# Kernel optimization log

Hardware: AMD Instinct MI355X
Metric: run time of the kernel (lower is better)

## Reference

```python
import jax, jax.numpy as jnp
import numpy as np

B, NA, NB, DF, H, DO, NT = 32, 128, 1024, 128, 512, 128, 5
NPAIR = NT * NT  # nn_index = z1*5 + z2 -> 25 pair-type MLPs


def setup_inputs() -> dict:
    key = jax.random.key(0)
    ks = jax.random.split(key, 6)
    z = jax.random.randint(ks[0], (B, NA), 0, NT)
    r = jax.random.normal(ks[1], (B, NA, 3), jnp.float32) * 5.0
    x = jax.random.normal(ks[2], (B, NA, DF), jnp.float32)
    t = jax.random.randint(ks[3], (B, NB, 2), 0, NA)
    pad = NB // 8  # last 1/8 of bonds are -1 padding, as in the torch module
    t = t.at[:, NB - pad:, :].set(-1)
    # Stacked per-pair-type 2-layer MLP params (map_list)
    W1 = jax.random.normal(ks[4], (NPAIR, 2 * DF, H), jnp.float32) / np.sqrt(2.0 * DF)
    b1 = jnp.zeros((NPAIR, H), jnp.float32)
    W2 = jax.random.normal(ks[5], (NPAIR, H, DO), jnp.float32) / np.sqrt(1.0 * H)
    b2 = jnp.zeros((NPAIR, DO), jnp.float32)
    return dict(z=z, r=r, x=x, t=t, W1=W1, b1=b1, W2=W2, b2=b2)


def reference(z, r, x, t, W1, b1, W2, b2):
    n_batch, n_bonds, _ = t.shape
    n_atoms = x.shape[1]
    x_f = x.reshape(-1, x.shape[-1])          # [B*NA, DF]
    z_f = z.reshape(-1)                        # [B*NA]
    r_f = r.reshape(-1, 3)                     # [B*NA, 3]
    offs = (jnp.arange(n_batch) * n_atoms)[:, None, None]
    valid = t[:, :, 0] != -1                   # [B, NB]
    tg = jnp.clip(t, 0, None) + offs           # global atom indices (padding clamped to 0)
    t1 = tg[:, :, 0].reshape(-1)
    t2 = tg[:, :, 1].reshape(-1)
    vmask = valid.reshape(-1)                  # [N] = [B*NB]
    # gather+concat pair features; zero out padded rows (masked_scatter into zeros)
    x_c = jnp.concatenate([x_f[t1], x_f[t2]], axis=1) * vmask[:, None].astype(x.dtype)
    z1 = z_f[t1]
    z2 = z_f[t2]
    nn_index = jnp.where(vmask, z1 * NT + z2, -1)
    # per-pair-type MLP dispatch (loop over fixed 25 types; rows selected by mask)
    y = jnp.zeros((x_c.shape[0], W2.shape[-1]), x.dtype)
    for i in range(NPAIR):
        h = jax.nn.silu(x_c @ W1[i] + b1[i])
        out_i = h @ W2[i] + b2[i]
        y = jnp.where((nn_index == i)[:, None], out_i, y)
    y = y.reshape(n_batch, n_bonds, -1)
    # normalized bond vectors, zeroed for padded bonds
    v = (r_f[t2] - r_f[t1]).reshape(n_batch, n_bonds, 3)
    n2 = jnp.sum(v * v, axis=2, keepdims=True)
    v = v / jnp.sqrt(jnp.clip(n2, 1e-24, None))  # == clamp(norm, 1e-12)
    v = v * valid[:, :, None].astype(v.dtype)
    return (z, x, t, y, v)
```

## Files before the change

### kernel.cpp

```cpp
#include <hip/hip_runtime.h>
#include <cstddef>
#include <cstdint>

#define NBATCH 32
#define NATOM  128
#define DFEAT  128
#define HDIM   512
#define DOUT   128
#define NTYPE  5
#define NPAIR  25
#define NBOND  32768
#define CAP    1408
#define TPT    22
#define GBLK   550

#define OFF_X 4096
#define OFF_T 528384
#define OFF_Y 593920
#define OFF_V 4788224

#define PRE_A 580
#define PRE_B 256
#define PRE_C 1600
#define PRE_D 800
#define PRE_BLK (PRE_A+PRE_B+PRE_C+PRE_D)

typedef __attribute__((ext_vector_type(8))) short short8;
typedef __attribute__((ext_vector_type(4))) short short4_t;
typedef __attribute__((ext_vector_type(4))) float f32x4;

#define GAS(x) ((__attribute__((address_space(1))) const void*)(x))
#define LAS(x) ((__attribute__((address_space(3))) void*)(x))

__device__ __forceinline__ unsigned short f2bf(float f) {
    unsigned u = __float_as_uint(f);
    u = (u + 0x7FFFu + ((u >> 16) & 1u)) >> 16;
    return (unsigned short)u;
}

__global__ __launch_bounds__(256) void k_pre(const int* __restrict__ z,
                                             const float* __restrict__ x,
                                             const int* __restrict__ t,
                                             const float* __restrict__ W1,
                                             const float* __restrict__ W2,
                                             float* __restrict__ out,
                                             short* __restrict__ x_bf,
                                             short* __restrict__ W1p,
                                             short* __restrict__ W2p,
                                             int* __restrict__ cursors) {
    int bid = blockIdx.x, tid = threadIdx.x;
    if (bid == 0 && tid < 32) cursors[tid] = 0;
    if (bid < PRE_A) {
        int i4 = (bid * 256 + tid) * 4;
        float4 o;
        if (i4 < OFF_X) {
            const int4 zi = *(const int4*)&z[i4];
            o = make_float4((float)zi.x, (float)zi.y, (float)zi.z, (float)zi.w);
        } else if (i4 < OFF_T) {
            o = *(const float4*)&x[i4 - OFF_X];
        } else {
            const int4 ti = *(const int4*)&t[i4 - OFF_T];
            o = make_float4((float)ti.x, (float)ti.y, (float)ti.z, (float)ti.w);
        }
        *(float4*)&out[i4] = o;
    } else if (bid < PRE_A + PRE_B) {
        int idx = (bid - PRE_A) * 256 + tid;
        const float4* px = (const float4*)&x[idx * 8];
        float4 fa = px[0], fb = px[1];
        short8 v;
        v[0]=(short)f2bf(fa.x); v[1]=(short)f2bf(fa.y); v[2]=(short)f2bf(fa.z); v[3]=(short)f2bf(fa.w);
        v[4]=(short)f2bf(fb.x); v[5]=(short)f2bf(fb.y); v[6]=(short)f2bf(fb.z); v[7]=(short)f2bf(fb.w);
        *((short8*)x_bf + idx) = v;
    } else if (bid < PRE_A + PRE_B + PRE_C) {
        int idx = (bid - PRE_A - PRE_B) * 256 + tid;
        int l  = idx & 63;
        int cf = (idx >> 6) & 31;
        int ks = (idx >> 11) & 7;
        int p  = idx >> 14;
        int col = cf*16 + (l & 15);
        int kb  = ks*32 + (l >> 4)*8;
        const float* src = W1 + ((size_t)p*2*DFEAT + kb)*HDIM + col;
        short8 v;
        #pragma unroll
        for (int j = 0; j < 8; ++j) v[j] = (short)f2bf(src[(size_t)j*HDIM]);
        __builtin_nontemporal_store(v, (short8*)W1p + idx);
    } else {
        int idx = (bid - PRE_A - PRE_B - PRE_C) * 256 + tid;
        int l  = idx & 63;
        int cf = (idx >> 6) & 7;
        int ks = (idx >> 9) & 15;
        int p  = idx >> 13;
        int col = cf*16 + (l & 15);
        int kb  = ks*32 + (l >> 4)*8;
        const float* src = W2 + ((size_t)p*HDIM + kb)*DOUT + col;
        short8 v;
        #pragma unroll
        for (int j = 0; j < 8; ++j) v[j] = (short)f2bf(src[(size_t)j*DOUT]);
        __builtin_nontemporal_store(v, (short8*)W2p + idx);
    }
}

__global__ __launch_bounds__(256) void k_scatter(const int* __restrict__ z,
                                                 const float* __restrict__ r,
                                                 const int* __restrict__ t,
                                                 float* __restrict__ out_v,
                                                 float* __restrict__ y_out,
                                                 int* __restrict__ cursors,
                                                 int* __restrict__ bond_ids) {
    __shared__ int hist[NPAIR];
    __shared__ int base[NPAIR];
    int tid = threadIdx.x;
    if (tid < NPAIR) hist[tid] = 0;
    __syncthreads();

    int i = blockIdx.x * 256 + tid;
    int b = i >> 10;
    int t1 = t[2*i], t2 = t[2*i+1];
    float vx = 0.f, vy = 0.f, vz = 0.f;
    int p = -1, rk = 0;
    if (t1 != -1) {
        int g1 = b*NATOM + t1, g2 = b*NATOM + t2;
        p = z[g1]*NTYPE + z[g2];
        rk = atomicAdd(&hist[p], 1);
        float dx = r[3*g2+0]-r[3*g1+0];
        float dy = r[3*g2+1]-r[3*g1+1];
        float dz = r[3*g2+2]-r[3*g1+2];
        float n2 = fmaxf(dx*dx+dy*dy+dz*dz, 1e-24f);
        float inv = 1.0f / sqrtf(n2);
        vx = dx*inv; vy = dy*inv; vz = dz*inv;
    } else {
        float4 zr = make_float4(0.f, 0.f, 0.f, 0.f);
        float4* yp = (float4*)&y_out[(size_t)i * DOUT];
        #pragma unroll
        for (int c = 0; c < DOUT/4; ++c) yp[c] = zr;
    }
    out_v[3*i+0] = vx; out_v[3*i+1] = vy; out_v[3*i+2] = vz;
    __syncthreads();
    if (tid < NPAIR) base[tid] = atomicAdd(&cursors[tid], hist[tid]);
    __syncthreads();
    if (p >= 0) {
        int pos = base[p] + rk;
        if (pos < CAP) bond_ids[p*CAP + pos] = i;
    }
}

__global__ __launch_bounds__(256, 2) void k_gemm(const short* __restrict__ x_bf,
                                                 const int* __restrict__ t,
                                                 const short* __restrict__ W1p,
                                                 const float* __restrict__ b1,
                                                 const short* __restrict__ W2p,
                                                 const float* __restrict__ b2,
                                                 const int* __restrict__ cursors,
                                                 const int* __restrict__ bond_ids,
                                                 float* __restrict__ y_out) {
    int orig = blockIdx.x;
    int xcd = orig & 7, ib = orig >> 3;
    int wk = (xcd < 6 ? xcd*69 : 414 + (xcd-6)*68) + ib;
    int p = wk / TPT, tileIdx = wk % TPT;
    int cnt = min(cursors[p], CAP);
    if (tileIdx*64 >= cnt) return;
    int nb = min(64, cnt - tileIdx*64);

    __shared__ short xs[64*256];
    __shared__ short hs[64*128];
    __shared__ char  wbuf[2*8192];
    __shared__ float b1s[HDIM];
    __shared__ float b2s[DOUT];
    __shared__ int   srow[64][2];
    __shared__ int   sb[64];

    int tid = threadIdx.x;
    int l = tid & 63, wc = tid >> 6;
    int lr = l & 15, lq = l >> 4;
    int klq = lq * 16;

    if (tid < 64) {
        int bi = (tid < nb) ? bond_ids[p*CAP + tileIdx*64 + tid] : -1;
        sb[tid] = bi;
        int r0 = 0, r1 = 0;
        if (bi >= 0) { int b = bi >> 10; r0 = b*NATOM + t[2*bi]; r1 = b*NATOM + t[2*bi+1]; }
        srow[tid][0] = r0; srow[tid][1] = r1;
    }
    if (tid < 128)
        __builtin_amdgcn_global_load_lds(GAS((const char*)(b1 + (size_t)p*HDIM) + tid*16),
                                         LAS((char*)b1s + tid*16), 16, 0, 0);
    if (tid < 32)
        __builtin_amdgcn_global_load_lds(GAS((const char*)(b2 + (size_t)p*DOUT) + tid*16),
                                         LAS((char*)b2s + tid*16), 16, 0, 0);
    {
        const char* s_ = (const char*)W1p + (((size_t)(p*8)*32 + wc*2)*64 + l)*16;
        char* d_ = wbuf + wc*2048 + l*16;
        __builtin_amdgcn_global_load_lds(GAS(s_), LAS(d_), 16, 0, 0);
        __builtin_amdgcn_global_load_lds(GAS(s_+1024), LAS(d_+1024), 16, 0, 0);
    }
    __syncthreads();

    #pragma unroll
    for (int j = 0; j < 8; ++j) {
        int o = j*4096 + tid*16;
        int row = o >> 9;
        int c16 = ((o >> 4) & 31) ^ (row & 7);
        const char* src = (const char*)x_bf + ((size_t)srow[row][c16 >> 4]*DFEAT + (c16 & 15)*8)*2;
        __builtin_amdgcn_global_load_lds(GAS(src), LAS((char*)xs + o), 16, 0, 0);
    }
    __syncthreads();

    f32x4 yacc[4][2] = {};

    for (int chunk = 0; chunk < 4; ++chunk) {
        float b1c0 = b1s[chunk*128 + wc*32 + lr];
        float b1c1 = b1s[chunk*128 + wc*32 + 16 + lr];
        f32x4 acc1[4][2] = {};
        #pragma unroll
        for (int ks = 0; ks < 8; ++ks) {
            if (ks < 7) {
                const char* s_ = (const char*)W1p + (((size_t)(p*8 + ks+1)*32 + chunk*8 + wc*2)*64 + l)*16;
                char* d_ = wbuf + ((ks+1)&1)*8192 + wc*2048 + l*16;
                __builtin_amdgcn_global_load_lds(GAS(s_), LAS(d_), 16, 0, 0);
                __builtin_amdgcn_global_load_lds(GAS(s_+1024), LAS(d_+1024), 16, 0, 0);
            } else {
                const char* s_ = (const char*)W2p + (((size_t)(p*16 + chunk*4)*8 + wc*2)*64 + l)*16;
                char* d_ = wbuf + wc*2048 + l*16;
                __builtin_amdgcn_global_load_lds(GAS(s_), LAS(d_), 16, 0, 0);
                __builtin_amdgcn_global_load_lds(GAS(s_+1024), LAS(d_+1024), 16, 0, 0);
            }
            asm volatile("s_waitcnt vmcnt(2)" ::: "memory");
            const char* wb = wbuf + (ks&1)*8192 + wc*2048 + l*16;
            short8 w0 = *(const short8*)wb;
            short8 w1 = *(const short8*)(wb + 1024);
            #pragma unroll
            for (int rf = 0; rf < 4; ++rf) {
                int row = rf*16 + lr;
                short8 a = *(const short8*)((const char*)xs + row*512 + ((ks*64 + klq) ^ ((row & 7) << 4)));
                acc1[rf][0] = __builtin_amdgcn_mfma_f32_16x16x32_bf16(a, w0, acc1[rf][0], 0, 0, 0);
                acc1[rf][1] = __builtin_amdgcn_mfma_f32_16x16x32_bf16(a, w1, acc1[rf][1], 0, 0, 0);
            }
        }
        #pragma unroll
        for (int rf = 0; rf < 4; ++rf) {
            #pragma unroll
            for (int cf = 0; cf < 2; ++cf) {
                int colb = (wc*32 + cf*16 + lr) * 2;
                float bb = cf ? b1c1 : b1c0;
                #pragma unroll
                for (int reg = 0; reg < 4; ++reg) {
                    int row = rf*16 + lq*4 + reg;
                    float sv = acc1[rf][cf][reg] + bb;
                    float hv = sv / (1.0f + __expf(-sv));
                    *(unsigned short*)((char*)hs + row*256 + (colb ^ ((row & 7) << 4))) = f2bf(hv);
                }
            }
        }
        asm volatile("s_waitcnt lgkmcnt(0)" ::: "memory");
        __builtin_amdgcn_s_barrier();

        #pragma unroll
        for (int s2 = 0; s2 < 4; ++s2) {
            if (s2 < 3) {
                const char* s_ = (const char*)W2p + (((size_t)(p*16 + chunk*4 + s2+1)*8 + wc*2)*64 + l)*16;
                char* d_ = wbuf + ((s2+1)&1)*8192 + wc*2048 + l*16;
                __builtin_amdgcn_global_load_lds(GAS(s_), LAS(d_), 16, 0, 0);
                __builtin_amdgcn_global_load_lds(GAS(s_+1024), LAS(d_+1024), 16, 0, 0);
            } else if (chunk < 3) {
                const char* s_ = (const char*)W1p + (((size_t)(p*8)*32 + (chunk+1)*8 + wc*2)*64 + l)*16;
                char* d_ = wbuf + wc*2048 + l*16;
                __builtin_amdgcn_global_load_lds(GAS(s_), LAS(d_), 16, 0, 0);
                __builtin_amdgcn_global_load_lds(GAS(s_+1024), LAS(d_+1024), 16, 0, 0);
            }
            if (chunk == 3 && s2 == 3) asm volatile("s_waitcnt vmcnt(0)" ::: "memory");
            else                       asm volatile("s_waitcnt vmcnt(2)" ::: "memory");
            const char* wb = wbuf + (s2&1)*8192 + wc*2048 + l*16;
            short8 w0 = *(const short8*)wb;
            short8 w1 = *(const short8*)(wb + 1024);
            #pragma unroll
            for (int rf = 0; rf < 4; ++rf) {
                int row = rf*16 + lr;
                short8 ha = *(const short8*)((const char*)hs + row*256 + ((s2*64 + klq) ^ ((row & 7) << 4)));
                yacc[rf][0] = __builtin_amdgcn_mfma_f32_16x16x32_bf16(ha, w0, yacc[rf][0], 0, 0, 0);
                yacc[rf][1] = __builtin_amdgcn_mfma_f32_16x16x32_bf16(ha, w1, yacc[rf][1], 0, 0, 0);
            }
        }
        if (chunk < 3) {
            asm volatile("s_waitcnt lgkmcnt(0)" ::: "memory");
            __builtin_amdgcn_s_barrier();
        }
    }

    float bo0 = b2s[wc*32 + lr], bo1 = b2s[wc*32 + 16 + lr];
    #pragma unroll
    for (int rf = 0; rf < 4; ++rf) {
        #pragma unroll
        for (int cf = 0; cf < 2; ++cf) {
            int col = wc*32 + cf*16 + lr;
            float bo = cf ? bo1 : bo0;
            #pragma unroll
            for (int reg = 0; reg < 4; ++reg) {
                int row = rf*16 + lq*4 + reg;
                if (row < nb)
                    y_out[(size_t)sb[row]*DOUT + col] = yacc[rf][cf][reg] + bo;
            }
        }
    }
}

extern "C" void kernel_launch(void* const* d_in, const int* in_sizes, int n_in,
                              void* d_out, int out_size, void* d_ws, size_t ws_size,
                              hipStream_t stream) {
    const int*   z  = (const int*)  d_in[0];
    const float* r  = (const float*)d_in[1];
    const float* x  = (const float*)d_in[2];
    const int*   t  = (const int*)  d_in[3];
    const float* W1 = (const float*)d_in[4];
    const float* b1 = (const float*)d_in[5];
    const float* W2 = (const float*)d_in[6];
    const float* b2 = (const float*)d_in[7];
    float* out = (float*)d_out;

    char* ws = (char*)d_ws;
    int*   cursors  = (int*)(ws);
    int*   bond_ids = (int*)(ws + 256);
    short* x_bf     = (short*)(ws + 141312);
    short* W1p      = (short*)(ws + 1189888);
    short* W2p      = (short*)(ws + 7743488);

    k_pre<<<PRE_BLK, 256, 0, stream>>>(z, x, t, W1, W2, out, x_bf, W1p, W2p, cursors);
    k_scatter<<<NBOND/256, 256, 0, stream>>>(z, r, t, out + OFF_V, out + OFF_Y, cursors, bond_ids);
    k_gemm<<<GBLK, 256, 0, stream>>>(x_bf, t, W1p, b1, W2p, b2, cursors, bond_ids, out + OFF_Y);
}
```

Baseline: 49.40 us.

## Triple-buffer weight staging, add L2 warm-up prefetch, hoist A-fragment loads

The weight-streaming pipeline moves from a double to a triple LDS buffer with prefetch distance two, driven by a unified STAGE macro that walks the W1 and W2 slices. Each tile first reads its share of its pair type's packed weights so the data sits in L2 for the other tiles of that type. A-fragment LDS reads are hoisted ahead of the wait, and the MFMA bursts are wrapped in s_setprio. Weight packing stores become regular stores so the packed weights stay cacheable. The extra LDS and warm-up reads may lower occupancy or add memory traffic.

```diff
diff --git a/kernel.cpp b/kernel.cpp
--- a/kernel.cpp
+++ b/kernel.cpp
@@ -26,7 +26,6 @@
 #define PRE_BLK (PRE_A+PRE_B+PRE_C+PRE_D)
 
 typedef __attribute__((ext_vector_type(8))) short short8;
-typedef __attribute__((ext_vector_type(4))) short short4_t;
 typedef __attribute__((ext_vector_type(4))) float f32x4;
 
 #define GAS(x) ((__attribute__((address_space(1))) const void*)(x))
@@ -83,7 +82,7 @@
         short8 v;
         #pragma unroll
         for (int j = 0; j < 8; ++j) v[j] = (short)f2bf(src[(size_t)j*HDIM]);
-        __builtin_nontemporal_store(v, (short8*)W1p + idx);
+        *((short8*)W1p + idx) = v;
     } else {
         int idx = (bid - PRE_A - PRE_B - PRE_C) * 256 + tid;
         int l  = idx & 63;
@@ -96,7 +95,7 @@
         short8 v;
         #pragma unroll
         for (int j = 0; j < 8; ++j) v[j] = (short)f2bf(src[(size_t)j*DOUT]);
-        __builtin_nontemporal_store(v, (short8*)W2p + idx);
+        *((short8*)W2p + idx) = v;
     }
 }
 
@@ -144,6 +143,17 @@
     }
 }
 
+#define STAGE(cc_, rr_) do { \
+    int _c = (cc_), _r = (rr_); \
+    if (_r >= 12) { _r -= 12; _c += 1; if (_c >= 4) _c = 0; } \
+    const char* _s; \
+    if (_r < 8) _s = (const char*)W1p + (((size_t)(p*8 + _r)*32 + _c*8 + wc*2)*64 + l)*16; \
+    else        _s = (const char*)W2p + (((size_t)(p*16 + _c*4 + (_r-8))*8 + wc*2)*64 + l)*16; \
+    char* _d = (char*)wbuf + ((rr_)%3)*8192 + wc*2048 + l*16; \
+    __builtin_amdgcn_global_load_lds(GAS(_s), LAS(_d), 16, 0, 0); \
+    __builtin_amdgcn_global_load_lds(GAS(_s+1024), LAS(_d+1024), 16, 0, 0); \
+} while(0)
+
 __global__ __launch_bounds__(256, 2) void k_gemm(const short* __restrict__ x_bf,
                                                  const int* __restrict__ t,
                                                  const short* __restrict__ W1p,
@@ -160,10 +170,11 @@
     int cnt = min(cursors[p], CAP);
     if (tileIdx*64 >= cnt) return;
     int nb = min(64, cnt - tileIdx*64);
+    int ntiles = (cnt + 63) >> 6;
 
     __shared__ short xs[64*256];
     __shared__ short hs[64*128];
-    __shared__ char  wbuf[2*8192];
+    __shared__ char  wbuf[3*8192];
     __shared__ float b1s[HDIM];
     __shared__ float b2s[DOUT];
     __shared__ int   srow[64][2];
@@ -181,18 +192,34 @@
         if (bi >= 0) { int b = bi >> 10; r0 = b*NATOM + t[2*bi]; r1 = b*NATOM + t[2*bi+1]; }
         srow[tid][0] = r0; srow[tid][1] = r1;
     }
+
+    {
+        float snk = 0.f;
+        const char* w1t = (const char*)W1p + (size_t)p*262144;
+        int o1 = (int)(((long)tileIdx * 262144) / ntiles) & ~63;
+        int e1 = (int)(((long)(tileIdx+1) * 262144) / ntiles);
+        for (int o = o1 + tid*16; o < e1; o += 4096) {
+            float4 v = *(const float4*)(w1t + o);
+            snk += v.x + v.y + v.z + v.w;
+        }
+        const char* w2t = (const char*)W2p + (size_t)p*131072;
+        int o2 = (int)(((long)tileIdx * 131072) / ntiles) & ~63;
+        int e2 = (int)(((long)(tileIdx+1) * 131072) / ntiles);
+        for (int o = o2 + tid*16; o < e2; o += 4096) {
+            float4 v = *(const float4*)(w2t + o);
+            snk += v.x + v.y + v.z + v.w;
+        }
+        asm volatile("" :: "v"(snk));
+    }
+
     if (tid < 128)
         __builtin_amdgcn_global_load_lds(GAS((const char*)(b1 + (size_t)p*HDIM) + tid*16),
                                          LAS((char*)b1s + tid*16), 16, 0, 0);
     if (tid < 32)
         __builtin_amdgcn_global_load_lds(GAS((const char*)(b2 + (size_t)p*DOUT) + tid*16),
                                          LAS((char*)b2s + tid*16), 16, 0, 0);
-    {
-        const char* s_ = (const char*)W1p + (((size_t)(p*8)*32 + wc*2)*64 + l)*16;
-        char* d_ = wbuf + wc*2048 + l*16;
-        __builtin_amdgcn_global_load_lds(GAS(s_), LAS(d_), 16, 0, 0);
-        __builtin_amdgcn_global_load_lds(GAS(s_+1024), LAS(d_+1024), 16, 0, 0);
-    }
+    STAGE(0, 0);
+    STAGE(0, 1);
     __syncthreads();
 
     #pragma unroll
@@ -207,34 +234,35 @@
 
     f32x4 yacc[4][2] = {};
 
-    for (int chunk = 0; chunk < 4; ++chunk) {
-        float b1c0 = b1s[chunk*128 + wc*32 + lr];
-        float b1c1 = b1s[chunk*128 + wc*32 + 16 + lr];
+    for (int c = 0; c < 4; ++c) {
+        float b1c0 = b1s[c*128 + wc*32 + lr];
+        float b1c1 = b1s[c*128 + wc*32 + 16 + lr];
         f32x4 acc1[4][2] = {};
         #pragma unroll
-        for (int ks = 0; ks < 8; ++ks) {
-            if (ks < 7) {
-                const char* s_ = (const char*)W1p + (((size_t)(p*8 + ks+1)*32 + chunk*8 + wc*2)*64 + l)*16;
-                char* d_ = wbuf + ((ks+1)&1)*8192 + wc*2048 + l*16;
-                __builtin_amdgcn_global_load_lds(GAS(s_), LAS(d_), 16, 0, 0);
-                __builtin_amdgcn_global_load_lds(GAS(s_+1024), LAS(d_+1024), 16, 0, 0);
-            } else {
-                const char* s_ = (const char*)W2p + (((size_t)(p*16 + chunk*4)*8 + wc*2)*64 + l)*16;
-                char* d_ = wbuf + wc*2048 + l*16;
-                __builtin_amdgcn_global_load_lds(GAS(s_), LAS(d_), 16, 0, 0);
-                __builtin_amdgcn_global_load_lds(GAS(s_+1024), LAS(d_+1024), 16, 0, 0);
+        for (int r = 0; r < 8; ++r) {
+            short8 a0, a1, a2, a3;
+            {
+                const char* xb = (const char*)xs;
+                a0 = *(const short8*)(xb + (0*16+lr)*512 + ((r*64 + klq) ^ (((0*16+lr)&7) << 4)));
+                a1 = *(const short8*)(xb + (1*16+lr)*512 + ((r*64 + klq) ^ (((1*16+lr)&7) << 4)));
+                a2 = *(const short8*)(xb + (2*16+lr)*512 + ((r*64 + klq) ^ (((2*16+lr)&7) << 4)));
+                a3 = *(const short8*)(xb + (3*16+lr)*512 + ((r*64 + klq) ^ (((3*16+lr)&7) << 4)));
             }
-            asm volatile("s_waitcnt vmcnt(2)" ::: "memory");
-            const char* wb = wbuf + (ks&1)*8192 + wc*2048 + l*16;
+            STAGE(c, r + 2);
+            asm volatile("s_waitcnt vmcnt(4)" ::: "memory");
+            const char* wb = (const char*)wbuf + (r%3)*8192 + wc*2048 + l*16;
             short8 w0 = *(const short8*)wb;
             short8 w1 = *(const short8*)(wb + 1024);
-            #pragma unroll
-            for (int rf = 0; rf < 4; ++rf) {
-                int row = rf*16 + lr;
-                short8 a = *(const short8*)((const char*)xs + row*512 + ((ks*64 + klq) ^ ((row & 7) << 4)));
-                acc1[rf][0] = __builtin_amdgcn_mfma_f32_16x16x32_bf16(a, w0, acc1[rf][0], 0, 0, 0);
-                acc1[rf][1] = __builtin_amdgcn_mfma_f32_16x16x32_bf16(a, w1, acc1[rf][1], 0, 0, 0);
-            }
+            __builtin_amdgcn_s_setprio(1);
+            acc1[0][0] = __builtin_amdgcn_mfma_f32_16x16x32_bf16(a0, w0, acc1[0][0], 0, 0, 0);
+            acc1[0][1] = __builtin_amdgcn_mfma_f32_16x16x32_bf16(a0, w1, acc1[0][1], 0, 0, 0);
+            acc1[1][0] = __builtin_amdgcn_mfma_f32_16x16x32_bf16(a1, w0, acc1[1][0], 0, 0, 0);
+            acc1[1][1] = __builtin_amdgcn_mfma_f32_16x16x32_bf16(a1, w1, acc1[1][1], 0, 0, 0);
+            acc1[2][0] = __builtin_amdgcn_mfma_f32_16x16x32_bf16(a2, w0, acc1[2][0], 0, 0, 0);
+            acc1[2][1] = __builtin_amdgcn_mfma_f32_16x16x32_bf16(a2, w1, acc1[2][1], 0, 0, 0);
+            acc1[3][0] = __builtin_amdgcn_mfma_f32_16x16x32_bf16(a3, w0, acc1[3][0], 0, 0, 0);
+            acc1[3][1] = __builtin_amdgcn_mfma_f32_16x16x32_bf16(a3, w1, acc1[3][1], 0, 0, 0);
+            __builtin_amdgcn_s_setprio(0);
         }
         #pragma unroll
         for (int rf = 0; rf < 4; ++rf) {
@@ -255,32 +283,33 @@
         __builtin_amdgcn_s_barrier();
 
         #pragma unroll
-        for (int s2 = 0; s2 < 4; ++s2) {
-            if (s2 < 3) {
-                const char* s_ = (const char*)W2p + (((size_t)(p*16 + chunk*4 + s2+1)*8 + wc*2)*64 + l)*16;
-                char* d_ = wbuf + ((s2+1)&1)*8192 + wc*2048 + l*16;
-                __builtin_amdgcn_global_load_lds(GAS(s_), LAS(d_), 16, 0, 0);
-                __builtin_amdgcn_global_load_lds(GAS(s_+1024), LAS(d_+1024), 16, 0, 0);
-            } else if (chunk < 3) {
-                const char* s_ = (const char*)W1p + (((size_t)(p*8)*32 + (chunk+1)*8 + wc*2)*64 + l)*16;
-                char* d_ = wbuf + wc*2048 + l*16;
-                __builtin_amdgcn_global_load_lds(GAS(s_), LAS(d_), 16, 0, 0);
-                __builtin_amdgcn_global_load_lds(GAS(s_+1024), LAS(d_+1024), 16, 0, 0);
+        for (int r2 = 8; r2 < 12; ++r2) {
+            short8 a0, a1, a2, a3;
+            {
+                const char* hb = (const char*)hs;
+                int s2 = r2 - 8;
+                a0 = *(const short8*)(hb + (0*16+lr)*256 + ((s2*64 + klq) ^ (((0*16+lr)&7) << 4)));
+                a1 = *(const short8*)(hb + (1*16+lr)*256 + ((s2*64 + klq) ^ (((1*16+lr)&7) << 4)));
+                a2 = *(const short8*)(hb + (2*16+lr)*256 + ((s2*64 + klq) ^ (((2*16+lr)&7) << 4)));
+                a3 = *(const short8*)(hb + (3*16+lr)*256 + ((s2*64 + klq) ^ (((3*16+lr)&7) << 4)));
             }
-            if (chunk == 3 && s2 == 3) asm volatile("s_waitcnt vmcnt(0)" ::: "memory");
-            else                       asm volatile("s_waitcnt vmcnt(2)" ::: "memory");
-            const char* wb = wbuf + (s2&1)*8192 + wc*2048 + l*16;
+            STAGE(c, r2 + 2);
+            asm volatile("s_waitcnt vmcnt(4)" ::: "memory");
+            const char* wb = (const char*)wbuf + (r2%3)*8192 + wc*2048 + l*16;
             short8 w0 = *(const short8*)wb;
             short8 w1 = *(const short8*)(wb + 1024);
-            #pragma unroll
-            for (int rf = 0; rf < 4; ++rf) {
-                int row = rf*16 + lr;
-                short8 ha = *(const short8*)((const char*)hs + row*256 + ((s2*64 + klq) ^ ((row & 7) << 4)));
-                yacc[rf][0] = __builtin_amdgcn_mfma_f32_16x16x32_bf16(ha, w0, yacc[rf][0], 0, 0, 0);
-                yacc[rf][1] = __builtin_amdgcn_mfma_f32_16x16x32_bf16(ha, w1, yacc[rf][1], 0, 0, 0);
-            }
-        }
-        if (chunk < 3) {
+            __builtin_amdgcn_s_setprio(1);
+            yacc[0][0] = __builtin_amdgcn_mfma_f32_16x16x32_bf16(a0, w0, yacc[0][0], 0, 0, 0);
+            yacc[0][1] = __builtin_amdgcn_mfma_f32_16x16x32_bf16(a0, w1, yacc[0][1], 0, 0, 0);
+            yacc[1][0] = __builtin_amdgcn_mfma_f32_16x16x32_bf16(a1, w0, yacc[1][0], 0, 0, 0);
+            yacc[1][1] = __builtin_amdgcn_mfma_f32_16x16x32_bf16(a1, w1, yacc[1][1], 0, 0, 0);
+            yacc[2][0] = __builtin_amdgcn_mfma_f32_16x16x32_bf16(a2, w0, yacc[2][0], 0, 0, 0);
+            yacc[2][1] = __builtin_amdgcn_mfma_f32_16x16x32_bf16(a2, w1, yacc[2][1], 0, 0, 0);
+            yacc[3][0] = __builtin_amdgcn_mfma_f32_16x16x32_bf16(a3, w0, yacc[3][0], 0, 0, 0);
+            yacc[3][1] = __builtin_amdgcn_mfma_f32_16x16x32_bf16(a3, w1, yacc[3][1], 0, 0, 0);
+            __builtin_amdgcn_s_setprio(0);
+        }
+        if (c < 3) {
             asm volatile("s_waitcnt lgkmcnt(0)" ::: "memory");
             __builtin_amdgcn_s_barrier();
         }
```

New measurement: 45.62 us, median of 3. 7.6% less time.
